# Kernel tuning notes

Hardware: AMD Instinct MI355X
Metric: run time of the kernel (lower is better)

The kernel has to match this reference:

```python
import jax, jax.numpy as jnp
import numpy as np

D_MODEL = 1024
D_STATE = 16
DT_RANK = 64  # d_model // 16 ('auto')
DT_MIN = 0.001
DT_MAX = 0.1


def setup_inputs() -> dict:
    key = jax.random.key(0)
    ks = jax.random.split(key, 7)
    B, S = 2, 2048
    return {
        "x": jax.random.normal(ks[0], (B, S, D_MODEL), jnp.float32),
        "w_in": jax.random.normal(ks[1], (D_MODEL, D_MODEL), jnp.float32) / np.sqrt(D_MODEL).astype(np.float32),
        "w_x": jax.random.normal(ks[2], (D_MODEL, DT_RANK + 2 * D_STATE), jnp.float32) / np.sqrt(D_MODEL).astype(np.float32),
        "w_dt": jax.random.normal(ks[3], (DT_RANK, D_MODEL), jnp.float32) / np.sqrt(DT_RANK).astype(np.float32),
        "b_dt": jnp.zeros((D_MODEL,), jnp.float32),
        "A_log": jax.random.normal(ks[5], (D_MODEL, D_STATE), jnp.float32) * 0.5,
        "Dp": jax.random.normal(ks[6], (D_MODEL,), jnp.float32),
    }


def reference(x, w_in, w_x, w_dt, b_dt, A_log, Dp):
    # x: (b, s, d)
    x_in = jnp.einsum('bsd,de->bse', x, w_in)          # in_proj, (b,s,d_inner=d)
    proj = jnp.einsum('bsd,dp->bsp', x_in, w_x)        # x_proj, (b,s,dt_rank+2n)
    dt_low, Bm, Cm = jnp.split(proj, [DT_RANK, DT_RANK + D_STATE], axis=-1)
    # dt_proj + softplus + range scaling -> (b,s,d)
    dt = jax.nn.softplus(jnp.einsum('bsr,rd->bsd', dt_low, w_dt) + b_dt) * (DT_MAX - DT_MIN) + DT_MIN
    A = -jnp.exp(A_log)                                # (d, n), strictly negative

    b, s, d = x.shape
    h0 = jnp.zeros((b, d, D_STATE), x.dtype)

    # time-major streams for scan
    dt_tm = jnp.swapaxes(dt, 0, 1)     # (s,b,d)
    u_tm = jnp.swapaxes(x_in, 0, 1)    # (s,b,d)
    B_tm = jnp.swapaxes(Bm, 0, 1)      # (s,b,n)
    C_tm = jnp.swapaxes(Cm, 0, 1)      # (s,b,n)

    def step(h, inp):
        dtt, ut, bt, ct = inp
        dA = dtt[:, :, None] * A                      # (b,d,n) = dt[b,d]*A[d,n]
        barA = jnp.exp(dA)
        # bar_B = dA; source sums the input term over channel dim d (keepdim)
        inp_term = jnp.einsum('bdn,bn,bd->bn', dA, bt, ut)  # (b,n)
        h = barA * h + inp_term[:, None, :]           # broadcast over d
        y = jnp.einsum('bdn,bn->bd', h, ct) + Dp * ut # (b,d)
        return h, y

    _, ys = jax.lax.scan(step, h0, (dt_tm, u_tm, B_tm, C_tm))  # ys: (s,b,d)
    return jnp.swapaxes(ys, 0, 1)                     # (b,s,d)
```

## Files before the change

### kernel.cpp

```cpp
#include <hip/hip_runtime.h>
#include <hip/hip_bf16.h>

#define D_MODEL 1024
#define D_STATE 16
#define DT_RANK 64
#define SEQ 2048
#define BATCH 2
#define M_TOTAL 4096
#define CHUNKS 64
#define CLEN 32

typedef __bf16 bf16x8 __attribute__((ext_vector_type(8)));
typedef float f32x4 __attribute__((ext_vector_type(4)));

__device__ __forceinline__ unsigned short f2bf(float f) {
    union { float f; unsigned int u; } v; v.f = f;
    unsigned int r = v.u + 0x7FFFu + ((v.u >> 16) & 1u);
    return (unsigned short)(r >> 16);
}
__device__ __forceinline__ float bf2f(unsigned short u) {
    union { unsigned int i; float f; } v; v.i = ((unsigned int)u) << 16; return v.f;
}
__device__ __forceinline__ void gload16(const void* g, void* l) {
    __builtin_amdgcn_global_load_lds(
        (const __attribute__((address_space(1))) unsigned int*)g,
        (__attribute__((address_space(3))) unsigned int*)l, 16, 0, 0);
}

__global__ void __launch_bounds__(256) k_setup(const float* __restrict__ x,
                                               const float* __restrict__ win,
                                               const float* __restrict__ wx,
                                               const float* __restrict__ alog,
                                               unsigned short* __restrict__ xb,
                                               unsigned short* __restrict__ wib,
                                               unsigned short* __restrict__ bt,
                                               unsigned short* __restrict__ wxT,
                                               unsigned short* __restrict__ wxBC,
                                               float* __restrict__ aneg) {
    __shared__ float tile[32][33];
    int blk = blockIdx.x;
    int t = threadIdx.x;
    if (blk < 4096) {
        int i = blk * 256 + t;
        float4 v = reinterpret_cast<const float4*>(x)[i];
        ushort4 o;
        o.x = f2bf(v.x); o.y = f2bf(v.y); o.z = f2bf(v.z); o.w = f2bf(v.w);
        reinterpret_cast<ushort4*>(xb)[i] = o;
    } else if (blk < 5120) {
        int i = (blk - 4096) * 256 + t;
        float4 v = reinterpret_cast<const float4*>(win)[i];
        ushort4 o;
        o.x = f2bf(v.x); o.y = f2bf(v.y); o.z = f2bf(v.z); o.w = f2bf(v.w);
        reinterpret_cast<ushort4*>(wib)[i] = o;
    } else if (blk < 6144) {
        int blk2 = blk - 5120;
        int bx = blk2 & 31, by = blk2 >> 5;
        int tx = t & 31, ty = t >> 5;
        int xc = bx * 32 + tx;
#pragma unroll
        for (int j = 0; j < 4; j++)
            tile[ty + 8 * j][tx] = win[(by * 32 + ty + 8 * j) * D_MODEL + xc];
        __syncthreads();
        int x2 = by * 32 + tx;
#pragma unroll
        for (int j = 0; j < 4; j++)
            bt[(bx * 32 + ty + 8 * j) * D_MODEL + x2] = f2bf(tile[tx][ty + 8 * j]);
    } else if (blk < 6400) {
        int idx = (blk - 6144) * 256 + t;
        int e = idx & 1023, p = idx >> 10;
        wxT[p * D_MODEL + e] = f2bf(wx[e * 96 + p]);
    } else if (blk < 6528) {
        int idx = (blk - 6400) * 256 + t;
        int e = idx & 1023, p = idx >> 10;
        wxBC[p * D_MODEL + e] = f2bf(wx[e * 96 + 64 + p]);
    } else {
        int i = (blk - 6528) * 256 + t;
        if (i < D_MODEL * D_STATE) aneg[i] = -expf(alog[i]);
    }
}

__global__ void __launch_bounds__(256) k_prepgemm(const unsigned short* __restrict__ wxT,
                                                  const unsigned short* __restrict__ wib,
                                                  float* __restrict__ Cp) {
    __shared__ unsigned short sA[2][64 * 32];
    __shared__ unsigned short sB[2][128 * 32];
    int bid = blockIdx.x;
    int n0 = (bid & 7) * 128;
    int ks = bid >> 3;
    int kbase = ks * 256;
    int t = threadIdx.x;
    int lane = t & 63;
    int w = t >> 6;
    int c = lane & 15, q = lane >> 4;

    const unsigned short* ga = wxT + (t >> 2) * D_MODEL + (t & 3) * 8 + kbase;
    const unsigned short* gb = wib + (n0 + (t >> 2)) * D_MODEL + (t & 3) * 8 + kbase;

    f32x4 acc[4][2] = {};
    {
        char* la = (char*)&sA[0][0] + w * 1024;
        char* lb = (char*)&sB[0][0] + w * 1024;
        gload16(ga, la);
        gload16(gb, lb);
        gload16(gb + 64 * D_MODEL, lb + 4096);
    }
    int cur = 0;
    for (int it = 0; it < 8; it++) {
        __syncthreads();
        if (it + 1 < 8) {
            int kn = (it + 1) * 32;
            char* la = (char*)&sA[cur ^ 1][0] + w * 1024;
            char* lb = (char*)&sB[cur ^ 1][0] + w * 1024;
            gload16(ga + kn, la);
            gload16(gb + kn, lb);
            gload16(gb + 64 * D_MODEL + kn, lb + 4096);
        }
        bf16x8 af[4], bfr[2];
#pragma unroll
        for (int i = 0; i < 4; i++)
            af[i] = *reinterpret_cast<const bf16x8*>(&sA[cur][(i * 16 + c) * 32 + q * 8]);
#pragma unroll
        for (int j = 0; j < 2; j++)
            bfr[j] = *reinterpret_cast<const bf16x8*>(&sB[cur][(w * 32 + j * 16 + c) * 32 + q * 8]);
#pragma unroll
        for (int i = 0; i < 4; i++)
#pragma unroll
            for (int j = 0; j < 2; j++)
                acc[i][j] = __builtin_amdgcn_mfma_f32_16x16x32_bf16(af[i], bfr[j], acc[i][j], 0, 0, 0);
        cur ^= 1;
    }
#pragma unroll
    for (int i = 0; i < 4; i++) {
        int p = i * 16 + q * 4;
#pragma unroll
        for (int j = 0; j < 2; j++) {
            int d = n0 + w * 32 + j * 16 + c;
#pragma unroll
            for (int r = 0; r < 4; r++)
                Cp[(ks * 64 + p + r) * D_MODEL + d] = acc[i][j][r];
        }
    }
}

__global__ void __launch_bounds__(256) k_prepreduce(const float* __restrict__ Cp,
                                                    float* __restrict__ Tt) {
    int idx = blockIdx.x * 256 + threadIdx.x;
    int d = idx & 1023;
    int p = idx >> 10;
    Tt[p * D_MODEL + d] = Cp[p * D_MODEL + d] + Cp[(64 + p) * D_MODEL + d] +
                          Cp[(128 + p) * D_MODEL + d] + Cp[(192 + p) * D_MODEL + d];
}

__global__ void __launch_bounds__(256) k_prep2(const float* __restrict__ wdt,
                                               const float* __restrict__ Tt,
                                               unsigned short* __restrict__ bt) {
    __shared__ float sw[DT_RANK][8];
    int m0 = blockIdx.x * 8;
    int tid = threadIdx.x;
    for (int s = tid; s < DT_RANK * 8; s += 256) {
        int r = s >> 3, rr = s & 7;
        sw[r][rr] = wdt[r * D_MODEL + m0 + rr];
    }
    __syncthreads();
    float acc[8][4] = {};
    for (int r = 0; r < DT_RANK; r++) {
        float tv0 = Tt[r * D_MODEL + tid];
        float tv1 = Tt[r * D_MODEL + tid + 256];
        float tv2 = Tt[r * D_MODEL + tid + 512];
        float tv3 = Tt[r * D_MODEL + tid + 768];
#pragma unroll
        for (int rr = 0; rr < 8; rr++) {
            float wv = sw[r][rr];
            acc[rr][0] = fmaf(wv, tv0, acc[rr][0]);
            acc[rr][1] = fmaf(wv, tv1, acc[rr][1]);
            acc[rr][2] = fmaf(wv, tv2, acc[rr][2]);
            acc[rr][3] = fmaf(wv, tv3, acc[rr][3]);
        }
    }
#pragma unroll
    for (int rr = 0; rr < 8; rr++)
#pragma unroll
        for (int i = 0; i < 4; i++)
            bt[(D_MODEL + m0 + rr) * D_MODEL + tid + i * 256] = f2bf(acc[rr][i]);
}

__global__ void __launch_bounds__(256) k_gemm_big(const unsigned short* __restrict__ xb,
                                                  const unsigned short* __restrict__ bt,
                                                  const float* __restrict__ bdt,
                                                  unsigned short* __restrict__ xinb,
                                                  unsigned short* __restrict__ dtb) {
    __shared__ unsigned short sA[2][128 * 64];
    __shared__ unsigned short sB[2][128 * 64];
    int bid = blockIdx.x;
    int m0 = (bid & 31) * 128;
    int nt = bid >> 5;
    int n0 = nt * 128;
    int t = threadIdx.x;
    int lane = t & 63;
    int w = t >> 6;
    int wm = (w >> 1) * 64, wn = (w & 1) * 64;
    int c = lane & 15, q = lane >> 4;

    const unsigned short* gA[4];
    const unsigned short* gB[4];
#pragma unroll
    for (int L = 0; L < 4; L++) {
        int s = L * 256 + t;
        int row = s >> 3, ch = (s & 7) ^ (row & 7);
        gA[L] = xb + (m0 + row) * D_MODEL + ch * 8;
        gB[L] = bt + (n0 + row) * D_MODEL + ch * 8;
    }

    f32x4 acc[4][4] = {};
    {
        char* la = (char*)&sA[0][0] + w * 1024;
        char* lb = (char*)&sB[0][0] + w * 1024;
#pragma unroll
        for (int L = 0; L < 4; L++) {
            gload16(gA[L], la + L * 4096);
            gload16(gB[L], lb + L * 4096);
        }
    }
    int cur = 0;
    for (int it = 0; it < 16; it++) {
        __syncthreads();
        if (it + 1 < 16) {
            int kn = (it + 1) * 64;
            char* la = (char*)&sA[cur ^ 1][0] + w * 1024;
            char* lb = (char*)&sB[cur ^ 1][0] + w * 1024;
#pragma unroll
            for (int L = 0; L < 4; L++) {
                gload16(gA[L] + kn, la + L * 4096);
                gload16(gB[L] + kn, lb + L * 4096);
            }
        }
#pragma unroll
        for (int kk = 0; kk < 2; kk++) {
            int perm = (((kk << 2) | q) ^ (c & 7)) << 3;
            bf16x8 af[4], bfr[4];
#pragma unroll
            for (int i = 0; i < 4; i++)
                af[i] = *reinterpret_cast<const bf16x8*>(&sA[cur][(wm + i * 16 + c) * 64 + perm]);
#pragma unroll
            for (int j = 0; j < 4; j++)
                bfr[j] = *reinterpret_cast<const bf16x8*>(&sB[cur][(wn + j * 16 + c) * 64 + perm]);
#pragma unroll
            for (int i = 0; i < 4; i++)
#pragma unroll
                for (int j = 0; j < 4; j++)
                    acc[i][j] = __builtin_amdgcn_mfma_f32_16x16x32_bf16(af[i], bfr[j], acc[i][j], 0, 0, 0);
        }
        cur ^= 1;
    }

    if (nt < 8) {
#pragma unroll
        for (int i = 0; i < 4; i++) {
            int row = m0 + wm + i * 16 + q * 4;
#pragma unroll
            for (int j = 0; j < 4; j++) {
                int col = n0 + wn + j * 16 + c;
#pragma unroll
                for (int r = 0; r < 4; r++)
                    xinb[(row + r) * D_MODEL + col] = f2bf(acc[i][j][r]);
            }
        }
    } else {
#pragma unroll
        for (int i = 0; i < 4; i++) {
            int row = m0 + wm + i * 16 + q * 4;
#pragma unroll
            for (int j = 0; j < 4; j++) {
                int dcol = n0 + wn + j * 16 + c - D_MODEL;
                float bv = bdt[dcol];
#pragma unroll
                for (int r = 0; r < 4; r++) {
                    float xv = acc[i][j][r] + bv;
                    float sp = fmaxf(xv, 0.f) + __logf(1.f + __expf(-fabsf(xv)));
                    dtb[(row + r) * D_MODEL + dcol] = f2bf(sp * 0.099f + 0.001f);
                }
            }
        }
    }
}

__global__ void __launch_bounds__(256) k_bc(const unsigned short* __restrict__ xinb,
                                            const unsigned short* __restrict__ wxBC,
                                            float* __restrict__ bcp) {
    int bid = blockIdx.x;
    int m0 = (bid & 31) * 128;
    int ks = bid >> 5;
    int kbase = ks * 256;
    int t = threadIdx.x;
    int lane = t & 63, w = t >> 6;
    int c = lane & 15, q = lane >> 4;
    int mw = m0 + w * 32;
    f32x4 acc[2][2] = {};
    const unsigned short* pa0 = xinb + (mw + c) * D_MODEL + kbase + q * 8;
    const unsigned short* pa1 = xinb + (mw + 16 + c) * D_MODEL + kbase + q * 8;
    const unsigned short* pb0 = wxBC + c * D_MODEL + kbase + q * 8;
    const unsigned short* pb1 = wxBC + (16 + c) * D_MODEL + kbase + q * 8;
#pragma unroll
    for (int k0 = 0; k0 < 256; k0 += 32) {
        bf16x8 a0 = *reinterpret_cast<const bf16x8*>(pa0 + k0);
        bf16x8 a1 = *reinterpret_cast<const bf16x8*>(pa1 + k0);
        bf16x8 b0 = *reinterpret_cast<const bf16x8*>(pb0 + k0);
        bf16x8 b1 = *reinterpret_cast<const bf16x8*>(pb1 + k0);
        acc[0][0] = __builtin_amdgcn_mfma_f32_16x16x32_bf16(a0, b0, acc[0][0], 0, 0, 0);
        acc[0][1] = __builtin_amdgcn_mfma_f32_16x16x32_bf16(a0, b1, acc[0][1], 0, 0, 0);
        acc[1][0] = __builtin_amdgcn_mfma_f32_16x16x32_bf16(a1, b0, acc[1][0], 0, 0, 0);
        acc[1][1] = __builtin_amdgcn_mfma_f32_16x16x32_bf16(a1, b1, acc[1][1], 0, 0, 0);
    }
#pragma unroll
    for (int i = 0; i < 2; i++) {
        int row = mw + i * 16 + q * 4;
#pragma unroll
        for (int j = 0; j < 2; j++) {
            int p = j * 16 + c;
#pragma unroll
            for (int r = 0; r < 4; r++)
                bcp[(ks * M_TOTAL + row + r) * 32 + p] = acc[i][j][r];
        }
    }
}

__global__ void __launch_bounds__(256) k_winp(const unsigned short* __restrict__ dtb,
                                              const unsigned short* __restrict__ xinb,
                                              const float* __restrict__ aneg,
                                              const float* __restrict__ bcp,
                                              float* __restrict__ bc,
                                              float* __restrict__ winp) {
    __shared__ float r0[16][17], r1[16][17];
    __shared__ float sb[2][32];
    int m = blockIdx.x * 2;
    int tid = threadIdx.x;
    int n = tid & 15, strip = tid >> 4;
    float a0 = 0.f, a1 = 0.f;
    int d0 = strip * 64;
    for (int dd = 0; dd < 64; dd += 4) {
        int d = d0 + dd;
        ushort4 t0 = *reinterpret_cast<const ushort4*>(dtb + m * D_MODEL + d);
        ushort4 u0 = *reinterpret_cast<const ushort4*>(xinb + m * D_MODEL + d);
        ushort4 t1 = *reinterpret_cast<const ushort4*>(dtb + (m + 1) * D_MODEL + d);
        ushort4 u1 = *reinterpret_cast<const ushort4*>(xinb + (m + 1) * D_MODEL + d);
        float av0 = aneg[(d + 0) * 16 + n];
        float av1 = aneg[(d + 1) * 16 + n];
        float av2 = aneg[(d + 2) * 16 + n];
        float av3 = aneg[(d + 3) * 16 + n];
        a0 = fmaf(bf2f(t0.x) * bf2f(u0.x), av0, a0);
        a0 = fmaf(bf2f(t0.y) * bf2f(u0.y), av1, a0);
        a0 = fmaf(bf2f(t0.z) * bf2f(u0.z), av2, a0);
        a0 = fmaf(bf2f(t0.w) * bf2f(u0.w), av3, a0);
        a1 = fmaf(bf2f(t1.x) * bf2f(u1.x), av0, a1);
        a1 = fmaf(bf2f(t1.y) * bf2f(u1.y), av1, a1);
        a1 = fmaf(bf2f(t1.z) * bf2f(u1.z), av2, a1);
        a1 = fmaf(bf2f(t1.w) * bf2f(u1.w), av3, a1);
    }
    r0[strip][n] = a0; r1[strip][n] = a1;
    if (tid < 64) {
        int row = m + (tid >> 5), p = tid & 31;
        float s = bcp[row * 32 + p] + bcp[(M_TOTAL + row) * 32 + p] +
                  bcp[(2 * M_TOTAL + row) * 32 + p] + bcp[(3 * M_TOTAL + row) * 32 + p];
        bc[row * 32 + p] = s;
        sb[tid >> 5][p] = s;
    }
    __syncthreads();
    for (int s = 8; s > 0; s >>= 1) {
        if (strip < s) {
            r0[strip][n] += r0[strip + s][n];
            r1[strip][n] += r1[strip + s][n];
        }
        __syncthreads();
    }
    if (tid < 16) winp[m * 16 + n] = sb[0][n] * r0[0][n];
    else if (tid < 32) winp[(m + 1) * 16 + n] = sb[1][n] * r1[0][n];
}

__global__ void __launch_bounds__(256) k_scan1(const unsigned short* __restrict__ dtb,
                                               const float* __restrict__ winp,
                                               const float* __restrict__ aneg,
                                               float* __restrict__ h_loc,
                                               float* __restrict__ dtsum) {
    __shared__ unsigned short s_dt[16][256];
    __shared__ float s_w[16][16];
    int dc = blockIdx.x & 3;
    int c = (blockIdx.x >> 2) & (CHUNKS - 1);
    int b = blockIdx.x >> 8;
    int tid = threadIdx.x;
    int d = dc * 256 + tid;
    float Ad[16];
    const float4* ar = reinterpret_cast<const float4*>(aneg + d * 16);
#pragma unroll
    for (int j = 0; j < 4; j++) {
        float4 a4 = ar[j];
        Ad[4 * j + 0] = a4.x; Ad[4 * j + 1] = a4.y;
        Ad[4 * j + 2] = a4.z; Ad[4 * j + 3] = a4.w;
    }
    float h[16];
#pragma unroll
    for (int n = 0; n < 16; n++) h[n] = 0.f;
    float dts = 0.f;

    int r8 = tid >> 5, col8 = (tid & 31) * 8;
    for (int t0 = 0; t0 < CLEN; t0 += 16) {
        __syncthreads();
        int rowbase = b * SEQ + c * CLEN + t0;
        *reinterpret_cast<uint4*>(&s_dt[r8][col8]) =
            *reinterpret_cast<const uint4*>(dtb + (rowbase + r8) * D_MODEL + dc * 256 + col8);
        *reinterpret_cast<uint4*>(&s_dt[8 + r8][col8]) =
            *reinterpret_cast<const uint4*>(dtb + (rowbase + 8 + r8) * D_MODEL + dc * 256 + col8);
        {
            int r = tid >> 4, n = tid & 15;
            s_w[r][n] = winp[(rowbase + r) * 16 + n];
        }
        __syncthreads();
        for (int r = 0; r < 16; r++) {
            float dtv = bf2f(s_dt[r][tid]);
            dts += dtv;
#pragma unroll
            for (int n = 0; n < 16; n++) {
                float ba = __expf(dtv * Ad[n]);
                h[n] = fmaf(ba, h[n], s_w[r][n]);
            }
        }
    }
    int base = ((b * CHUNKS + c) * D_MODEL + d) * 16;
#pragma unroll
    for (int j = 0; j < 4; j++) {
        f32x4 v = {h[4 * j], h[4 * j + 1], h[4 * j + 2], h[4 * j + 3]};
        *reinterpret_cast<f32x4*>(h_loc + base + 4 * j) = v;
    }
    dtsum[(b * CHUNKS + c) * D_MODEL + d] = dts;
}

__global__ void __launch_bounds__(256) k_scan2(float* __restrict__ h_inout,
                                               const float* __restrict__ dtsum,
                                               const float* __restrict__ aneg) {
    int idx = blockIdx.x * 256 + threadIdx.x;
    int n = idx & 15;
    int d = (idx >> 4) & (D_MODEL - 1);
    int b = idx >> 14;
    float A = aneg[d * 16 + n];
    float H = 0.f;
    int off = (b * CHUNKS) * D_MODEL + d;
    float hl = h_inout[off * 16 + n];
    float ds = dtsum[off];
    for (int c = 0; c < CHUNKS; c++) {
        int off2 = off + D_MODEL;
        float hl_n = 0.f, ds_n = 0.f;
        if (c + 1 < CHUNKS) { hl_n = h_inout[off2 * 16 + n]; ds_n = dtsum[off2]; }
        float P = __expf(ds * A);
        h_inout[off * 16 + n] = H;
        H = fmaf(P, H, hl);
        hl = hl_n; ds = ds_n; off = off2;
    }
}

__global__ void __launch_bounds__(256) k_scan3(const unsigned short* __restrict__ dtb,
                                               const unsigned short* __restrict__ xinb,
                                               const float* __restrict__ winp,
                                               const float* __restrict__ bc,
                                               const float* __restrict__ aneg,
                                               const float* __restrict__ dp,
                                               const float* __restrict__ H_in,
                                               float* __restrict__ out) {
    __shared__ unsigned short s_dt[16][256], s_u[16][256];
    __shared__ float s_w[16][16], s_c[16][16];
    int dc = blockIdx.x & 3;
    int c = (blockIdx.x >> 2) & (CHUNKS - 1);
    int b = blockIdx.x >> 8;
    int tid = threadIdx.x;
    int d = dc * 256 + tid;
    float Ad[16];
    const float4* ar = reinterpret_cast<const float4*>(aneg + d * 16);
#pragma unroll
    for (int j = 0; j < 4; j++) {
        float4 a4 = ar[j];
        Ad[4 * j + 0] = a4.x; Ad[4 * j + 1] = a4.y;
        Ad[4 * j + 2] = a4.z; Ad[4 * j + 3] = a4.w;
    }
    float Dpd = dp[d];
    float h[16];
    int base = ((b * CHUNKS + c) * D_MODEL + d) * 16;
#pragma unroll
    for (int j = 0; j < 4; j++) {
        f32x4 v = *reinterpret_cast<const f32x4*>(H_in + base + 4 * j);
        h[4 * j] = v[0]; h[4 * j + 1] = v[1]; h[4 * j + 2] = v[2]; h[4 * j + 3] = v[3];
    }

    int r8 = tid >> 5, col8 = (tid & 31) * 8;
    for (int t0 = 0; t0 < CLEN; t0 += 16) {
        __syncthreads();
        int rowbase = b * SEQ + c * CLEN + t0;
        *reinterpret_cast<uint4*>(&s_dt[r8][col8]) =
            *reinterpret_cast<const uint4*>(dtb + (rowbase + r8) * D_MODEL + dc * 256 + col8);
        *reinterpret_cast<uint4*>(&s_dt[8 + r8][col8]) =
            *reinterpret_cast<const uint4*>(dtb + (rowbase + 8 + r8) * D_MODEL + dc * 256 + col8);
        *reinterpret_cast<uint4*>(&s_u[r8][col8]) =
            *reinterpret_cast<const uint4*>(xinb + (rowbase + r8) * D_MODEL + dc * 256 + col8);
        *reinterpret_cast<uint4*>(&s_u[8 + r8][col8]) =
            *reinterpret_cast<const uint4*>(xinb + (rowbase + 8 + r8) * D_MODEL + dc * 256 + col8);
        {
            int r = tid >> 4, n = tid & 15;
            s_w[r][n] = winp[(rowbase + r) * 16 + n];
            s_c[r][n] = bc[(rowbase + r) * 32 + 16 + n];
        }
        __syncthreads();
        for (int r = 0; r < 16; r++) {
            float dtv = bf2f(s_dt[r][tid]), uv = bf2f(s_u[r][tid]);
            float y = Dpd * uv;
#pragma unroll
            for (int n = 0; n < 16; n++) {
                float ba = __expf(dtv * Ad[n]);
                h[n] = fmaf(ba, h[n], s_w[r][n]);
                y = fmaf(h[n], s_c[r][n], y);
            }
            out[(rowbase + r) * D_MODEL + d] = y;
        }
    }
}

extern "C" void kernel_launch(void* const* d_in, const int* in_sizes, int n_in,
                              void* d_out, int out_size, void* d_ws, size_t ws_size,
                              hipStream_t stream) {
    const float* x     = (const float*)d_in[0];
    const float* w_in  = (const float*)d_in[1];
    const float* w_x   = (const float*)d_in[2];
    const float* w_dt  = (const float*)d_in[3];
    const float* b_dt  = (const float*)d_in[4];
    const float* A_log = (const float*)d_in[5];
    const float* Dp    = (const float*)d_in[6];
    float* out = (float*)d_out;

    char* ws = (char*)d_ws;
    unsigned short* xb   = (unsigned short*)(ws + 0);
    unsigned short* bt   = (unsigned short*)(ws + 8388608);
    float* Tt            = (float*)(ws + 12845056);
    float* aneg          = (float*)(ws + 13107200);
    float* bc            = (float*)(ws + 13172736);
    float* winp          = (float*)(ws + 13697024);
    unsigned short* xinb = (unsigned short*)(ws + 13959168);
    unsigned short* dtb  = (unsigned short*)(ws + 22347776);
    unsigned short* wib  = (unsigned short*)(ws + 22347776);
    unsigned short* wxT  = (unsigned short*)(ws + 24444928);
    float* Cp            = (float*)(ws + 24707072);
    unsigned short* wxBC = (unsigned short*)(ws + 30736384);
    float* bcp           = (float*)(ws + 30801920);
    float* h_loc         = (float*)(ws + 0);
    float* dtsum         = (float*)(ws + 8388608);

    k_setup<<<6592, 256, 0, stream>>>(x, w_in, w_x, A_log, xb, wib, bt, wxT, wxBC, aneg);
    k_prepgemm<<<32, 256, 0, stream>>>(wxT, wib, Cp);
    k_prepreduce<<<256, 256, 0, stream>>>(Cp, Tt);
    k_prep2<<<128, 256, 0, stream>>>(w_dt, Tt, bt);
    k_gemm_big<<<512, 256, 0, stream>>>(xb, bt, b_dt, xinb, dtb);
    k_bc<<<128, 256, 0, stream>>>(xinb, wxBC, bcp);
    k_winp<<<2048, 256, 0, stream>>>(dtb, xinb, aneg, bcp, bc, winp);
    k_scan1<<<BATCH * CHUNKS * 4, 256, 0, stream>>>(dtb, winp, aneg, h_loc, dtsum);
    k_scan2<<<128, 256, 0, stream>>>(h_loc, dtsum, aneg);
    k_scan3<<<BATCH * CHUNKS * 4, 256, 0, stream>>>(dtb, xinb, winp, bc, aneg, Dp, h_loc, out);
}
```

Measured before the change: 188.6 us.

## Fuse input-term reduction into B/C projection GEMM using MFMA with transposed A

The scalar k_winp reduction of dt*u*A over channels is replaced by an MFMA product of the elementwise dt*u tile with a bf16 transposed copy of A, computed inside the B/C projection kernel and sharing its xin loads. A small k_fin kernel then sums the split-K partials and forms winp. This is meant to remove the 2048-block scalar reduction pass and its re-read of dtb, xinb and aneg. In exchange, A is rounded to bf16 and dt*u is rounded before accumulation, which lowers precision. There is also extra partial-sum traffic through the new wpp buffer.

```diff
diff --git a/kernel.cpp b/kernel.cpp
--- a/kernel.cpp
+++ b/kernel.cpp
@@ -36,7 +36,8 @@
                                                unsigned short* __restrict__ bt,
                                                unsigned short* __restrict__ wxT,
                                                unsigned short* __restrict__ wxBC,
-                                               float* __restrict__ aneg) {
+                                               float* __restrict__ aneg,
+                                               unsigned short* __restrict__ anegT) {
     __shared__ float tile[32][33];
     int blk = blockIdx.x;
     int t = threadIdx.x;
@@ -75,7 +76,9 @@
         wxBC[p * D_MODEL + e] = f2bf(wx[e * 96 + 64 + p]);
     } else {
         int i = (blk - 6528) * 256 + t;
-        if (i < D_MODEL * D_STATE) aneg[i] = -expf(alog[i]);
+        float v = -expf(alog[i]);
+        aneg[i] = v;
+        anegT[(i & 15) * D_MODEL + (i >> 4)] = f2bf(v);
     }
 }
 
@@ -284,9 +287,12 @@
     }
 }
 
-__global__ void __launch_bounds__(256) k_bc(const unsigned short* __restrict__ xinb,
-                                            const unsigned short* __restrict__ wxBC,
-                                            float* __restrict__ bcp) {
+__global__ void __launch_bounds__(256) k_bcw(const unsigned short* __restrict__ xinb,
+                                             const unsigned short* __restrict__ dtb,
+                                             const unsigned short* __restrict__ wxBC,
+                                             const unsigned short* __restrict__ anegT,
+                                             float* __restrict__ bcp,
+                                             float* __restrict__ wpp) {
     int bid = blockIdx.x;
     int m0 = (bid & 31) * 128;
     int ks = bid >> 5;
@@ -295,21 +301,36 @@
     int lane = t & 63, w = t >> 6;
     int c = lane & 15, q = lane >> 4;
     int mw = m0 + w * 32;
-    f32x4 acc[2][2] = {};
+    f32x4 accb[2][2] = {};
+    f32x4 accw[2] = {};
     const unsigned short* pa0 = xinb + (mw + c) * D_MODEL + kbase + q * 8;
-    const unsigned short* pa1 = xinb + (mw + 16 + c) * D_MODEL + kbase + q * 8;
+    const unsigned short* pa1 = pa0 + 16 * D_MODEL;
+    const unsigned short* pt0 = dtb + (mw + c) * D_MODEL + kbase + q * 8;
+    const unsigned short* pt1 = pt0 + 16 * D_MODEL;
     const unsigned short* pb0 = wxBC + c * D_MODEL + kbase + q * 8;
-    const unsigned short* pb1 = wxBC + (16 + c) * D_MODEL + kbase + q * 8;
+    const unsigned short* pb1 = pb0 + 16 * D_MODEL;
+    const unsigned short* pA = anegT + c * D_MODEL + kbase + q * 8;
 #pragma unroll
     for (int k0 = 0; k0 < 256; k0 += 32) {
         bf16x8 a0 = *reinterpret_cast<const bf16x8*>(pa0 + k0);
         bf16x8 a1 = *reinterpret_cast<const bf16x8*>(pa1 + k0);
+        bf16x8 t0 = *reinterpret_cast<const bf16x8*>(pt0 + k0);
+        bf16x8 t1 = *reinterpret_cast<const bf16x8*>(pt1 + k0);
         bf16x8 b0 = *reinterpret_cast<const bf16x8*>(pb0 + k0);
         bf16x8 b1 = *reinterpret_cast<const bf16x8*>(pb1 + k0);
-        acc[0][0] = __builtin_amdgcn_mfma_f32_16x16x32_bf16(a0, b0, acc[0][0], 0, 0, 0);
-        acc[0][1] = __builtin_amdgcn_mfma_f32_16x16x32_bf16(a0, b1, acc[0][1], 0, 0, 0);
-        acc[1][0] = __builtin_amdgcn_mfma_f32_16x16x32_bf16(a1, b0, acc[1][0], 0, 0, 0);
-        acc[1][1] = __builtin_amdgcn_mfma_f32_16x16x32_bf16(a1, b1, acc[1][1], 0, 0, 0);
+        bf16x8 bA = *reinterpret_cast<const bf16x8*>(pA + k0);
+        bf16x8 g0, g1;
+#pragma unroll
+        for (int e = 0; e < 8; e++) {
+            g0[e] = (__bf16)((float)t0[e] * (float)a0[e]);
+            g1[e] = (__bf16)((float)t1[e] * (float)a1[e]);
+        }
+        accb[0][0] = __builtin_amdgcn_mfma_f32_16x16x32_bf16(a0, b0, accb[0][0], 0, 0, 0);
+        accb[0][1] = __builtin_amdgcn_mfma_f32_16x16x32_bf16(a0, b1, accb[0][1], 0, 0, 0);
+        accb[1][0] = __builtin_amdgcn_mfma_f32_16x16x32_bf16(a1, b0, accb[1][0], 0, 0, 0);
+        accb[1][1] = __builtin_amdgcn_mfma_f32_16x16x32_bf16(a1, b1, accb[1][1], 0, 0, 0);
+        accw[0] = __builtin_amdgcn_mfma_f32_16x16x32_bf16(g0, bA, accw[0], 0, 0, 0);
+        accw[1] = __builtin_amdgcn_mfma_f32_16x16x32_bf16(g1, bA, accw[1], 0, 0, 0);
     }
 #pragma unroll
     for (int i = 0; i < 2; i++) {
@@ -319,61 +340,28 @@
             int p = j * 16 + c;
 #pragma unroll
             for (int r = 0; r < 4; r++)
-                bcp[(ks * M_TOTAL + row + r) * 32 + p] = acc[i][j][r];
-        }
-    }
-}
-
-__global__ void __launch_bounds__(256) k_winp(const unsigned short* __restrict__ dtb,
-                                              const unsigned short* __restrict__ xinb,
-                                              const float* __restrict__ aneg,
-                                              const float* __restrict__ bcp,
-                                              float* __restrict__ bc,
-                                              float* __restrict__ winp) {
-    __shared__ float r0[16][17], r1[16][17];
-    __shared__ float sb[2][32];
-    int m = blockIdx.x * 2;
-    int tid = threadIdx.x;
-    int n = tid & 15, strip = tid >> 4;
-    float a0 = 0.f, a1 = 0.f;
-    int d0 = strip * 64;
-    for (int dd = 0; dd < 64; dd += 4) {
-        int d = d0 + dd;
-        ushort4 t0 = *reinterpret_cast<const ushort4*>(dtb + m * D_MODEL + d);
-        ushort4 u0 = *reinterpret_cast<const ushort4*>(xinb + m * D_MODEL + d);
-        ushort4 t1 = *reinterpret_cast<const ushort4*>(dtb + (m + 1) * D_MODEL + d);
-        ushort4 u1 = *reinterpret_cast<const ushort4*>(xinb + (m + 1) * D_MODEL + d);
-        float av0 = aneg[(d + 0) * 16 + n];
-        float av1 = aneg[(d + 1) * 16 + n];
-        float av2 = aneg[(d + 2) * 16 + n];
-        float av3 = aneg[(d + 3) * 16 + n];
-        a0 = fmaf(bf2f(t0.x) * bf2f(u0.x), av0, a0);
-        a0 = fmaf(bf2f(t0.y) * bf2f(u0.y), av1, a0);
-        a0 = fmaf(bf2f(t0.z) * bf2f(u0.z), av2, a0);
-        a0 = fmaf(bf2f(t0.w) * bf2f(u0.w), av3, a0);
-        a1 = fmaf(bf2f(t1.x) * bf2f(u1.x), av0, a1);
-        a1 = fmaf(bf2f(t1.y) * bf2f(u1.y), av1, a1);
-        a1 = fmaf(bf2f(t1.z) * bf2f(u1.z), av2, a1);
-        a1 = fmaf(bf2f(t1.w) * bf2f(u1.w), av3, a1);
-    }
-    r0[strip][n] = a0; r1[strip][n] = a1;
-    if (tid < 64) {
-        int row = m + (tid >> 5), p = tid & 31;
-        float s = bcp[row * 32 + p] + bcp[(M_TOTAL + row) * 32 + p] +
-                  bcp[(2 * M_TOTAL + row) * 32 + p] + bcp[(3 * M_TOTAL + row) * 32 + p];
-        bc[row * 32 + p] = s;
-        sb[tid >> 5][p] = s;
-    }
-    __syncthreads();
-    for (int s = 8; s > 0; s >>= 1) {
-        if (strip < s) {
-            r0[strip][n] += r0[strip + s][n];
-            r1[strip][n] += r1[strip + s][n];
-        }
-        __syncthreads();
-    }
-    if (tid < 16) winp[m * 16 + n] = sb[0][n] * r0[0][n];
-    else if (tid < 32) winp[(m + 1) * 16 + n] = sb[1][n] * r1[0][n];
+                bcp[(ks * M_TOTAL + row + r) * 32 + p] = accb[i][j][r];
+        }
+#pragma unroll
+        for (int r = 0; r < 4; r++)
+            wpp[(ks * M_TOTAL + row + r) * 16 + c] = accw[i][r];
+    }
+}
+
+__global__ void __launch_bounds__(256) k_fin(const float* __restrict__ bcp,
+                                             const float* __restrict__ wpp,
+                                             float* __restrict__ bc,
+                                             float* __restrict__ winp) {
+    int idx = blockIdx.x * 256 + threadIdx.x;
+    int row = idx >> 5, p = idx & 31;
+    float s = bcp[row * 32 + p] + bcp[(M_TOTAL + row) * 32 + p] +
+              bcp[(2 * M_TOTAL + row) * 32 + p] + bcp[(3 * M_TOTAL + row) * 32 + p];
+    bc[row * 32 + p] = s;
+    if (p < 16) {
+        float wsum = wpp[row * 16 + p] + wpp[(M_TOTAL + row) * 16 + p] +
+                     wpp[(2 * M_TOTAL + row) * 16 + p] + wpp[(3 * M_TOTAL + row) * 16 + p];
+        winp[row * 16 + p] = s * wsum;
+    }
 }
 
 __global__ void __launch_bounds__(256) k_scan1(const unsigned short* __restrict__ dtb,
@@ -546,16 +534,18 @@
     float* Cp            = (float*)(ws + 24707072);
     unsigned short* wxBC = (unsigned short*)(ws + 30736384);
     float* bcp           = (float*)(ws + 30801920);
+    float* wpp           = (float*)(ws + 32899072);
+    unsigned short* anegT= (unsigned short*)(ws + 33947648);
     float* h_loc         = (float*)(ws + 0);
     float* dtsum         = (float*)(ws + 8388608);
 
-    k_setup<<<6592, 256, 0, stream>>>(x, w_in, w_x, A_log, xb, wib, bt, wxT, wxBC, aneg);
+    k_setup<<<6592, 256, 0, stream>>>(x, w_in, w_x, A_log, xb, wib, bt, wxT, wxBC, aneg, anegT);
     k_prepgemm<<<32, 256, 0, stream>>>(wxT, wib, Cp);
     k_prepreduce<<<256, 256, 0, stream>>>(Cp, Tt);
     k_prep2<<<128, 256, 0, stream>>>(w_dt, Tt, bt);
     k_gemm_big<<<512, 256, 0, stream>>>(xb, bt, b_dt, xinb, dtb);
-    k_bc<<<128, 256, 0, stream>>>(xinb, wxBC, bcp);
-    k_winp<<<2048, 256, 0, stream>>>(dtb, xinb, aneg, bcp, bc, winp);
+    k_bcw<<<128, 256, 0, stream>>>(xinb, dtb, wxBC, anegT, bcp, wpp);
+    k_fin<<<512, 256, 0, stream>>>(bcp, wpp, bc, winp);
     k_scan1<<<BATCH * CHUNKS * 4, 256, 0, stream>>>(dtb, winp, aneg, h_loc, dtsum);
     k_scan2<<<128, 256, 0, stream>>>(h_loc, dtsum, aneg);
     k_scan3<<<BATCH * CHUNKS * 4, 256, 0, stream>>>(dtb, xinb, winp, bc, aneg, Dp, h_loc, out);
```

Result: faster. 176.6 us (-6.3%).
